# Kernel optimization log

Measured on AMD Instinct MI355X. Metric: run time of the kernel, lower is better.

Reference implementation:

```python
import jax, jax.numpy as jnp
import numpy as np

NUM_HEADS = 4
HEAD_DIM = 64  # hidden_dim // num_heads = 256 // 4
NEG_SLOPE = 0.2


def setup_inputs() -> dict:
    key0 = jax.random.key(0)
    ks = jax.random.split(key0, 8)
    B, N, QD, VD = 32, 8192, 256, 256
    HD = NUM_HEADS * HEAD_DIM  # 256
    s_in = 1.0 / np.sqrt(QD)
    s_v = 1.0 / np.sqrt(VD)
    s_a = 1.0 / np.sqrt(HEAD_DIM)
    return {
        "query": jax.random.normal(ks[0], (B, QD), jnp.float32),
        "key": jax.random.normal(ks[1], (B, N, QD), jnp.float32),
        "value": jax.random.normal(ks[2], (B, N, VD), jnp.float32),
        # linear_query == linear_key (shared_weights=True)
        "Wq": jax.random.uniform(ks[3], (QD, HD), jnp.float32, -s_in, s_in),
        "bq": jax.random.uniform(ks[4], (HD,), jnp.float32, -s_in, s_in),
        # node_projection
        "Wv": jax.random.uniform(ks[5], (VD, HD), jnp.float32, -s_v, s_v),
        "bv": jax.random.uniform(ks[6], (HD,), jnp.float32, -s_v, s_v),
        # attention: Linear(head_dim, 1, bias=False)
        "a": jax.random.uniform(ks[7], (HEAD_DIM,), jnp.float32, -s_a, s_a),
    }


def reference(query, key, value, Wq, bq, Wv, bv, a):
    B, N, _ = key.shape
    H, D = NUM_HEADS, HEAD_DIM
    # projections (shared query/key weights)
    hq = (query @ Wq + bq).reshape(B, 1, H, D)          # [B,1,H,D]
    hk = (key @ Wq + bq).reshape(B, N, H, D)            # [B,N,H,D]
    hv = (value @ Wv + bv).reshape(B, N, H, D)          # [B,N,H,D]
    # additive attention score: leaky_relu(broadcast add) projected to scalar per head
    e = jax.nn.leaky_relu(hq + hk, negative_slope=NEG_SLOPE)  # [B,N,H,D]
    e = jnp.einsum('bnhd,d->bnh', e, a)                 # [B,N,H]
    # dropout=0.0 (eval) -> identity; softmax over nodes
    e = jax.nn.softmax(e, axis=1)                       # [B,N,H]
    scored = jnp.einsum('bnh,bnhf->bhf', e, hv)         # [B,H,D]
    h_prime = jax.nn.relu(scored.reshape(B, H * D))     # [B,H*D] (is_concat)
    return h_prime, e
```

## Files before the change

kernel.cpp:

```cpp
#include <hip/hip_runtime.h>
#include <hip/hip_bf16.h>

#define NUM_HEADS 4
#define HD 256
#define QD 256
#define VD 256
#define B_SZ 32
#define N_NODES 8192
#define NEG_SLOPE 0.2f
#define CH 32
#define NCH 32
#define KSTRIDE 1040

typedef short bf16x8 __attribute__((ext_vector_type(8)));
typedef float f32x4 __attribute__((ext_vector_type(4)));

static __device__ __forceinline__ unsigned short f2bf(float f) {
    __hip_bfloat16 h = __float2bfloat16(f);
    return *reinterpret_cast<unsigned short*>(&h);
}

static __device__ __forceinline__ void gload_lds16(const float* g, void* l) {
    __builtin_amdgcn_global_load_lds(
        (const __attribute__((address_space(1))) void*)g,
        (__attribute__((address_space(3))) void*)l, 16, 0, 0);
}

__global__ __launch_bounds__(256)
void prep_kernel(const float* __restrict__ query,
                 const float* __restrict__ Wq,
                 const float* __restrict__ bq,
                 unsigned short* __restrict__ WqP,
                 float* __restrict__ hqb) {
    int blk = blockIdx.x;
    int tid = threadIdx.x;
    if (blk < 32) {
        int b = blk, col = tid;
        float acc = 2.0f * bq[col];
#pragma unroll 16
        for (int k = 0; k < QD; ++k)
            acc += query[b * QD + k] * Wq[k * HD + col];
        hqb[b * HD + col] = acc;
    } else {
        int idx = blk - 32;
        int kstep = idx >> 2, g = idx & 3;
        int col = tid;
        int h = col >> 6, ct = (col >> 4) & 3, col16 = col & 15;
        unsigned short v[8];
#pragma unroll
        for (int j = 0; j < 8; ++j)
            v[j] = f2bf(Wq[(kstep * 32 + g * 8 + j) * HD + col]);
        *reinterpret_cast<uint4*>(
            WqP + kstep * 8192 + h * 2048 + ct * 512 + (g * 16 + col16) * 8) =
            *reinterpret_cast<uint4*>(v);
    }
}

__global__ __launch_bounds__(512, 2)
void fused_kernel(const float* __restrict__ key,
                  const float* __restrict__ value,
                  const unsigned short* __restrict__ WqP,
                  const float* __restrict__ hqb,
                  const float* __restrict__ avec,
                  float* __restrict__ s,
                  float* __restrict__ p_part,
                  float* __restrict__ pml) {
    __shared__ __align__(16) char smem[2 * (CH * KSTRIDE) + 2 * (CH * 1024)];

    char* kb0 = smem;
    char* kb1 = smem + CH * KSTRIDE;
    char* vb0 = smem + 2 * CH * KSTRIDE;
    char* vb1 = vb0 + CH * 1024;

    int bid = blockIdx.x;
    int b = bid >> 3, strip = bid & 7;
    int tid = threadIdx.x;
    int w = tid >> 6, lane = tid & 63;
    int col16 = lane & 15, g = (lane >> 4) & 3;
    int h = w & 3, half = w >> 2;
    int rowbase0 = strip * 1024;

    bf16x8 bfr[8][4];
    {
        const unsigned short* wp0 = WqP + h * 2048 + (g * 16 + col16) * 8;
#pragma unroll
        for (int ks = 0; ks < 8; ++ks)
#pragma unroll
            for (int ct = 0; ct < 4; ++ct)
                bfr[ks][ct] = *reinterpret_cast<const bf16x8*>(wp0 + ks * 8192 + ct * 512);
    }
    float av16[4][4], hq16[4][4];
#pragma unroll
    for (int ct = 0; ct < 4; ++ct)
#pragma unroll
        for (int r = 0; r < 4; ++r) {
            int d = ct * 16 + g * 4 + r;
            av16[ct][r] = avec[d];
            hq16[ct][r] = hqb[b * HD + h * 64 + d];
        }

    {
        int dummy = 0;
        float fd = 0.f;
#pragma unroll
        for (int ks = 0; ks < 8; ++ks)
#pragma unroll
            for (int ct = 0; ct < 4; ++ct)
                dummy ^= (int)bfr[ks][ct][0];
#pragma unroll
        for (int ct = 0; ct < 4; ++ct)
#pragma unroll
            for (int r = 0; r < 4; ++r)
                fd += av16[ct][r] + hq16[ct][r];
        asm volatile("" :: "v"(dummy), "v"(fd));
    }

    float mr = -1e30f, lr = 0.f;
    f32x4 pa = (f32x4){0.f, 0.f, 0.f, 0.f};

    {
        int rb = rowbase0;
#pragma unroll
        for (int r = 0; r < 4; ++r) {
            int lr_ = w * 4 + r;
            gload_lds16(key + ((size_t)(b * N_NODES + rb + lr_)) * QD + lane * 4,
                        kb0 + lr_ * KSTRIDE);
        }
#pragma unroll
        for (int r = 0; r < 4; ++r) {
            int lr_ = w * 4 + r;
            gload_lds16(value + ((size_t)(b * N_NODES + rb + lr_)) * VD + lane * 4,
                        vb0 + lr_ * 1024);
        }
    }

    for (int t = 0; t < NCH; ++t) {
        __builtin_amdgcn_s_barrier();
        if (t + 1 < NCH) {
            char* kbn = ((t + 1) & 1) ? kb1 : kb0;
            char* vbn = ((t + 1) & 1) ? vb1 : vb0;
            int rb = rowbase0 + (t + 1) * CH;
#pragma unroll
            for (int r = 0; r < 4; ++r) {
                int lr_ = w * 4 + r;
                gload_lds16(key + ((size_t)(b * N_NODES + rb + lr_)) * QD + lane * 4,
                            kbn + lr_ * KSTRIDE);
            }
#pragma unroll
            for (int r = 0; r < 4; ++r) {
                int lr_ = w * 4 + r;
                gload_lds16(value + ((size_t)(b * N_NODES + rb + lr_)) * VD + lane * 4,
                            vbn + lr_ * 1024);
            }
            if (t == 0) asm volatile("s_waitcnt vmcnt(8)" ::: "memory");
            else        asm volatile("s_waitcnt vmcnt(9)" ::: "memory");
        } else {
            asm volatile("s_waitcnt vmcnt(0)" ::: "memory");
        }
        __builtin_amdgcn_s_barrier();
        __builtin_amdgcn_sched_barrier(0);

        const char* kb = (t & 1) ? kb1 : kb0;
        const char* vb = (t & 1) ? vb1 : vb0;
        int n0c = rowbase0 + t * CH;

        bf16x8 a[8];
        {
            int krow = half * 16 + col16;
#pragma unroll
            for (int ks = 0; ks < 8; ++ks) {
                f32x4 lo = *reinterpret_cast<const f32x4*>(kb + krow * KSTRIDE + ks * 128 + g * 32);
                f32x4 hi = *reinterpret_cast<const f32x4*>(kb + krow * KSTRIDE + ks * 128 + g * 32 + 16);
                unsigned int u0, u1, u2, u3;
                asm("v_cvt_pk_bf16_f32 %0, %1, %2" : "=v"(u0) : "v"(lo[0]), "v"(lo[1]));
                asm("v_cvt_pk_bf16_f32 %0, %1, %2" : "=v"(u1) : "v"(lo[2]), "v"(lo[3]));
                asm("v_cvt_pk_bf16_f32 %0, %1, %2" : "=v"(u2) : "v"(hi[0]), "v"(hi[1]));
                asm("v_cvt_pk_bf16_f32 %0, %1, %2" : "=v"(u3) : "v"(hi[2]), "v"(hi[3]));
                uint4 tt = {u0, u1, u2, u3};
                a[ks] = *reinterpret_cast<bf16x8*>(&tt);
            }
        }

        f32x4 acc[4];
#pragma unroll
        for (int ct = 0; ct < 4; ++ct) acc[ct] = (f32x4){0.f, 0.f, 0.f, 0.f};
#pragma unroll
        for (int ks = 0; ks < 8; ++ks)
#pragma unroll
            for (int ct = 0; ct < 4; ++ct)
                acc[ct] = __builtin_amdgcn_mfma_f32_16x16x32_bf16(bfr[ks][ct], a[ks], acc[ct], 0, 0, 0);

        float dot = 0.f;
#pragma unroll
        for (int ct = 0; ct < 4; ++ct) {
#pragma unroll
            for (int r = 0; r < 4; ++r) {
                float pre = acc[ct][r] + hq16[ct][r];
                float tv = fmaxf(pre, NEG_SLOPE * pre);
                dot += av16[ct][r] * tv;
            }
        }
        dot += __shfl_xor(dot, 16, 64);
        dot += __shfl_xor(dot, 32, 64);

        if (lane < 16) {
            s[((size_t)(b * NUM_HEADS + h)) * N_NODES + n0c + half * 16 + lane] = dot;
        }

        float mc = dot;
        mc = fmaxf(mc, __shfl_xor(mc, 1, 64));
        mc = fmaxf(mc, __shfl_xor(mc, 2, 64));
        mc = fmaxf(mc, __shfl_xor(mc, 4, 64));
        mc = fmaxf(mc, __shfl_xor(mc, 8, 64));
        float mnew = fmaxf(mr, mc);
        float ep = __expf(dot - mnew);
        float lc = ep;
        lc += __shfl_xor(lc, 1, 64);
        lc += __shfl_xor(lc, 2, 64);
        lc += __shfl_xor(lc, 4, 64);
        lc += __shfl_xor(lc, 8, 64);
        float scf = __expf(mr - mnew);
        pa *= scf;
        lr = lr * scf + lc;
        mr = mnew;

#pragma unroll
        for (int n = 0; n < 16; ++n) {
            f32x4 v = *reinterpret_cast<const f32x4*>(vb + (half * 16 + n) * 1024 + lane * 16);
            float e = __shfl(ep, n, 64);
            pa += e * v;
        }
    }

    int slot = bid * 8 + w;
    *reinterpret_cast<f32x4*>(p_part + (size_t)slot * 256 + lane * 4) = pa;
    if (lane == 0) {
        pml[slot * 2] = mr;
        pml[slot * 2 + 1] = lr;
    }
}

__global__ __launch_bounds__(256)
void final_kernel(const float* __restrict__ p_part,
                  const float* __restrict__ pml,
                  const float* __restrict__ Wv,
                  const float* __restrict__ bv,
                  float* __restrict__ hout,
                  float* __restrict__ sc) {
    int bh = blockIdx.x;
    int b = bh >> 2, h = bh & 3;
    int tid = threadIdx.x;

    int slots[16];
    float mv[16], lv[16];
    float M = -1e30f;
#pragma unroll
    for (int i = 0; i < 16; ++i) {
        int strip = i >> 1, hf = i & 1;
        slots[i] = (b * 8 + strip) * 8 + hf * 4 + h;
        mv[i] = pml[slots[i] * 2];
        lv[i] = pml[slots[i] * 2 + 1];
        M = fmaxf(M, mv[i]);
    }
    float L = 0.f, acc = 0.f;
#pragma unroll
    for (int i = 0; i < 16; ++i) {
        float wf = __expf(mv[i] - M);
        L += wf * lv[i];
        acc += wf * p_part[(size_t)slots[i] * 256 + tid];
    }
    float invL = 1.0f / L;
    if (tid == 0) {
        sc[bh * 2] = M;
        sc[bh * 2 + 1] = invL;
    }
    __shared__ float ps[256];
    ps[tid] = acc * invL;
    __syncthreads();

    int d = tid & 63, kr = tid >> 6;
    float a2 = 0.f;
#pragma unroll 8
    for (int k = kr * 64; k < kr * 64 + 64; ++k)
        a2 += ps[k] * Wv[k * HD + h * 64 + d];
    __shared__ float rs[4][64];
    rs[kr][d] = a2;
    __syncthreads();
    if (tid < 64) {
        float o = bv[h * 64 + tid] + rs[0][tid] + rs[1][tid] + rs[2][tid] + rs[3][tid];
        hout[b * HD + h * 64 + tid] = fmaxf(o, 0.f);
    }
}

__global__ __launch_bounds__(256)
void epass_kernel(const float* __restrict__ s,
                  const float* __restrict__ sc,
                  float* __restrict__ e_out) {
    int bid = blockIdx.x;
    int b = bid >> 5, t = bid & 31;
    int n = t * 256 + threadIdx.x;
    float4 ev;
#pragma unroll
    for (int h = 0; h < 4; ++h) {
        float M = sc[(b * 4 + h) * 2];
        float invL = sc[(b * 4 + h) * 2 + 1];
        float sv = s[((size_t)(b * 4 + h)) * N_NODES + n];
        (&ev.x)[h] = __expf(sv - M) * invL;
    }
    *reinterpret_cast<float4*>(e_out + ((size_t)(b * N_NODES + n)) * 4) = ev;
}

extern "C" void kernel_launch(void* const* d_in, const int* in_sizes, int n_in,
                              void* d_out, int out_size, void* d_ws, size_t ws_size,
                              hipStream_t stream) {
    const float* query = (const float*)d_in[0];
    const float* key   = (const float*)d_in[1];
    const float* value = (const float*)d_in[2];
    const float* Wq    = (const float*)d_in[3];
    const float* bq    = (const float*)d_in[4];
    const float* Wv    = (const float*)d_in[5];
    const float* bv    = (const float*)d_in[6];
    const float* avec  = (const float*)d_in[7];
    float* out = (float*)d_out;

    char* ws = (char*)d_ws;
    unsigned short* WqP = (unsigned short*)ws;
    float* hqb    = (float*)(ws + 131072);
    float* s      = (float*)(ws + 163840);
    float* pml    = (float*)(ws + 4358144);
    float* sc     = (float*)(ws + 4374528);
    float* p_part = (float*)(ws + 4378624);

    prep_kernel<<<64, 256, 0, stream>>>(query, Wq, bq, WqP, hqb);
    fused_kernel<<<256, 512, 0, stream>>>(key, value, WqP, hqb, avec, s, p_part, pml);
    final_kernel<<<B_SZ * NUM_HEADS, 256, 0, stream>>>(p_part, pml, Wv, bv, out, sc);
    epass_kernel<<<B_SZ * 32, 256, 0, stream>>>(s, sc, out + B_SZ * HD);
}
```

Before: 128.2 us.

## Halve chunk size and use three-slot LDS ring with prefetch distance two

Shrinks each streamed chunk from 32 to 16 rows and replaces the key/value double buffer with a three-slot LDS ring, issuing loads two chunks ahead with adjusted vmcnt waits. The aim is to keep more global loads in flight and hide memory latency in this bandwidth-bound stream. Both wave halves now compute scores for the same 16 rows, so score MFMA work is duplicated. Each half masks to its own 8 rows for the online softmax and the value accumulation. The partial-slot indexing is rewritten but maps to the same per-wave slots.

```diff
diff --git a/kernel.cpp b/kernel.cpp
--- a/kernel.cpp
+++ b/kernel.cpp
@@ -8,9 +8,11 @@
 #define B_SZ 32
 #define N_NODES 8192
 #define NEG_SLOPE 0.2f
-#define CH 32
-#define NCH 32
+#define CH 16
+#define NCH 64
 #define KSTRIDE 1040
+#define SLOTSZ (CH * KSTRIDE + CH * 1024)
+#define RING 3
 
 typedef short bf16x8 __attribute__((ext_vector_type(8)));
 typedef float f32x4 __attribute__((ext_vector_type(4)));
@@ -65,12 +67,7 @@
                   float* __restrict__ s,
                   float* __restrict__ p_part,
                   float* __restrict__ pml) {
-    __shared__ __align__(16) char smem[2 * (CH * KSTRIDE) + 2 * (CH * 1024)];
-
-    char* kb0 = smem;
-    char* kb1 = smem + CH * KSTRIDE;
-    char* vb0 = smem + 2 * CH * KSTRIDE;
-    char* vb1 = vb0 + CH * 1024;
+    __shared__ __align__(16) char smem[RING * SLOTSZ];
 
     int bid = blockIdx.x;
     int b = bid >> 3, strip = bid & 7;
@@ -98,7 +95,6 @@
             av16[ct][r] = avec[d];
             hq16[ct][r] = hqb[b * HD + h * 64 + d];
         }
-
     {
         int dummy = 0;
         float fd = 0.f;
@@ -118,67 +114,71 @@
     float mr = -1e30f, lr = 0.f;
     f32x4 pa = (f32x4){0.f, 0.f, 0.f, 0.f};
 
-    {
-        int rb = rowbase0;
-#pragma unroll
-        for (int r = 0; r < 4; ++r) {
-            int lr_ = w * 4 + r;
+#pragma unroll
+    for (int pc = 0; pc < 2; ++pc) {
+        char* kslot = smem + pc * SLOTSZ;
+        char* vslot = kslot + CH * KSTRIDE;
+        int rb = rowbase0 + pc * CH;
+#pragma unroll
+        for (int r = 0; r < 2; ++r) {
+            int lr_ = w * 2 + r;
             gload_lds16(key + ((size_t)(b * N_NODES + rb + lr_)) * QD + lane * 4,
-                        kb0 + lr_ * KSTRIDE);
-        }
-#pragma unroll
-        for (int r = 0; r < 4; ++r) {
-            int lr_ = w * 4 + r;
+                        kslot + lr_ * KSTRIDE);
+        }
+#pragma unroll
+        for (int r = 0; r < 2; ++r) {
+            int lr_ = w * 2 + r;
             gload_lds16(value + ((size_t)(b * N_NODES + rb + lr_)) * VD + lane * 4,
-                        vb0 + lr_ * 1024);
+                        vslot + lr_ * 1024);
         }
     }
 
     for (int t = 0; t < NCH; ++t) {
         __builtin_amdgcn_s_barrier();
-        if (t + 1 < NCH) {
-            char* kbn = ((t + 1) & 1) ? kb1 : kb0;
-            char* vbn = ((t + 1) & 1) ? vb1 : vb0;
-            int rb = rowbase0 + (t + 1) * CH;
-#pragma unroll
-            for (int r = 0; r < 4; ++r) {
-                int lr_ = w * 4 + r;
+        if (t + 2 < NCH) {
+            int sl = (t + 2) % RING;
+            char* kslot = smem + sl * SLOTSZ;
+            char* vslot = kslot + CH * KSTRIDE;
+            int rb = rowbase0 + (t + 2) * CH;
+#pragma unroll
+            for (int r = 0; r < 2; ++r) {
+                int lr_ = w * 2 + r;
                 gload_lds16(key + ((size_t)(b * N_NODES + rb + lr_)) * QD + lane * 4,
-                            kbn + lr_ * KSTRIDE);
+                            kslot + lr_ * KSTRIDE);
             }
 #pragma unroll
-            for (int r = 0; r < 4; ++r) {
-                int lr_ = w * 4 + r;
+            for (int r = 0; r < 2; ++r) {
+                int lr_ = w * 2 + r;
                 gload_lds16(value + ((size_t)(b * N_NODES + rb + lr_)) * VD + lane * 4,
-                            vbn + lr_ * 1024);
+                            vslot + lr_ * 1024);
             }
             if (t == 0) asm volatile("s_waitcnt vmcnt(8)" ::: "memory");
             else        asm volatile("s_waitcnt vmcnt(9)" ::: "memory");
+        } else if (t + 2 == NCH) {
+            asm volatile("s_waitcnt vmcnt(5)" ::: "memory");
         } else {
             asm volatile("s_waitcnt vmcnt(0)" ::: "memory");
         }
         __builtin_amdgcn_s_barrier();
         __builtin_amdgcn_sched_barrier(0);
 
-        const char* kb = (t & 1) ? kb1 : kb0;
-        const char* vb = (t & 1) ? vb1 : vb0;
+        int sl = t % RING;
+        const char* kb = smem + sl * SLOTSZ;
+        const char* vb = kb + CH * KSTRIDE;
         int n0c = rowbase0 + t * CH;
 
         bf16x8 a[8];
-        {
-            int krow = half * 16 + col16;
-#pragma unroll
-            for (int ks = 0; ks < 8; ++ks) {
-                f32x4 lo = *reinterpret_cast<const f32x4*>(kb + krow * KSTRIDE + ks * 128 + g * 32);
-                f32x4 hi = *reinterpret_cast<const f32x4*>(kb + krow * KSTRIDE + ks * 128 + g * 32 + 16);
-                unsigned int u0, u1, u2, u3;
-                asm("v_cvt_pk_bf16_f32 %0, %1, %2" : "=v"(u0) : "v"(lo[0]), "v"(lo[1]));
-                asm("v_cvt_pk_bf16_f32 %0, %1, %2" : "=v"(u1) : "v"(lo[2]), "v"(lo[3]));
-                asm("v_cvt_pk_bf16_f32 %0, %1, %2" : "=v"(u2) : "v"(hi[0]), "v"(hi[1]));
-                asm("v_cvt_pk_bf16_f32 %0, %1, %2" : "=v"(u3) : "v"(hi[2]), "v"(hi[3]));
-                uint4 tt = {u0, u1, u2, u3};
-                a[ks] = *reinterpret_cast<bf16x8*>(&tt);
-            }
+#pragma unroll
+        for (int ks = 0; ks < 8; ++ks) {
+            f32x4 lo = *reinterpret_cast<const f32x4*>(kb + col16 * KSTRIDE + ks * 128 + g * 32);
+            f32x4 hi = *reinterpret_cast<const f32x4*>(kb + col16 * KSTRIDE + ks * 128 + g * 32 + 16);
+            unsigned int u0, u1, u2, u3;
+            asm("v_cvt_pk_bf16_f32 %0, %1, %2" : "=v"(u0) : "v"(lo[0]), "v"(lo[1]));
+            asm("v_cvt_pk_bf16_f32 %0, %1, %2" : "=v"(u1) : "v"(lo[2]), "v"(lo[3]));
+            asm("v_cvt_pk_bf16_f32 %0, %1, %2" : "=v"(u2) : "v"(hi[0]), "v"(hi[1]));
+            asm("v_cvt_pk_bf16_f32 %0, %1, %2" : "=v"(u3) : "v"(hi[2]), "v"(hi[3]));
+            uint4 tt = {u0, u1, u2, u3};
+            a[ks] = *reinterpret_cast<bf16x8*>(&tt);
         }
 
         f32x4 acc[4];
@@ -203,17 +203,17 @@
         dot += __shfl_xor(dot, 16, 64);
         dot += __shfl_xor(dot, 32, 64);
 
-        if (lane < 16) {
-            s[((size_t)(b * NUM_HEADS + h)) * N_NODES + n0c + half * 16 + lane] = dot;
-        }
-
-        float mc = dot;
+        if (lane < 16)
+            s[((size_t)(b * NUM_HEADS + h)) * N_NODES + n0c + lane] = dot;
+
+        float mydot = ((col16 >> 3) == half) ? dot : -1e30f;
+        float mc = mydot;
         mc = fmaxf(mc, __shfl_xor(mc, 1, 64));
         mc = fmaxf(mc, __shfl_xor(mc, 2, 64));
         mc = fmaxf(mc, __shfl_xor(mc, 4, 64));
         mc = fmaxf(mc, __shfl_xor(mc, 8, 64));
         float mnew = fmaxf(mr, mc);
-        float ep = __expf(dot - mnew);
+        float ep = __expf(mydot - mnew);
         float lc = ep;
         lc += __shfl_xor(lc, 1, 64);
         lc += __shfl_xor(lc, 2, 64);
@@ -225,14 +225,15 @@
         mr = mnew;
 
 #pragma unroll
-        for (int n = 0; n < 16; ++n) {
-            f32x4 v = *reinterpret_cast<const f32x4*>(vb + (half * 16 + n) * 1024 + lane * 16);
-            float e = __shfl(ep, n, 64);
+        for (int n = 0; n < 8; ++n) {
+            int row = half * 8 + n;
+            f32x4 v = *reinterpret_cast<const f32x4*>(vb + row * 1024 + lane * 16);
+            float e = __shfl(ep, row, 64);
             pa += e * v;
         }
     }
 
-    int slot = bid * 8 + w;
+    int slot = bid * 8 + half * 4 + h;
     *reinterpret_cast<f32x4*>(p_part + (size_t)slot * 256 + lane * 4) = pa;
     if (lane == 0) {
         pml[slot * 2] = mr;
```

Result: slower. 150.7 us (+17.6%).
